# Kernel tuning notes

Hardware: AMD Instinct MI355X
Metric: run time of the kernel (lower is better)

Reference implementation:

```python
import jax, jax.numpy as jnp
import numpy as np

N_WORD = 32000
N_CLASS = 5
N_HIDDEN = 32
T, B = 2048, 512

def setup_inputs() -> dict:
    key = jax.random.key(0)
    k_x, k_emb, k_w, k_b, k_cw, k_cb = jax.random.split(key, 6)
    x = jax.random.randint(k_x, (T, B), 0, N_WORD, dtype=jnp.int64 if jax.config.read('jax_enable_x64') else jnp.int32)
    s_emb = 1.0  # nn.Embedding default N(0,1)
    emb = jax.random.normal(k_emb, (N_WORD, N_HIDDEN), dtype=jnp.float32) * s_emb
    # nn.Linear default init: U(-1/sqrt(fan_in), 1/sqrt(fan_in))
    lim_rnn = 1.0 / np.sqrt(2 * N_HIDDEN)
    W_rnn = jax.random.uniform(k_w, (2 * N_HIDDEN, N_HIDDEN), jnp.float32, -lim_rnn, lim_rnn)
    b_rnn = jax.random.uniform(k_b, (N_HIDDEN,), jnp.float32, -lim_rnn, lim_rnn)
    lim_cls = 1.0 / np.sqrt(N_HIDDEN)
    W_cls = jax.random.uniform(k_cw, (N_HIDDEN, N_CLASS), jnp.float32, -lim_cls, lim_cls)
    b_cls = jax.random.uniform(k_cb, (N_CLASS,), jnp.float32, -lim_cls, lim_cls)
    return {"x": x, "emb": emb, "W_rnn": W_rnn, "b_rnn": b_rnn, "W_cls": W_cls, "b_cls": b_cls}

def reference(x, emb, W_rnn, b_rnn, W_cls, b_cls):
    # x: [T, B] int token ids. Embed -> [T, B, H]
    xe = emb[x]
    # Split W_rnn into the part applied to x_t and the part applied to h
    # (cat([xt, h]) @ W == xt @ W[:H] + h @ W[H:]), avoids per-step concat.
    Wx, Wh = W_rnn[:N_HIDDEN], W_rnn[N_HIDDEN:]
    h0 = jnp.zeros((x.shape[1], N_HIDDEN), dtype=emb.dtype)

    def step(h, xt):
        h = jnp.tanh(xt @ Wx + h @ Wh + b_rnn)
        return h, None

    h_final, _ = jax.lax.scan(step, h0, xe)
    y = h_final @ W_cls + b_cls  # [B, n_class]
    return y
```

## Files before the change

### kernel.cpp

```cpp
#include <hip/hip_runtime.h>
#include <hip/hip_bf16.h>

#define TT 2048
#define BB 512
#define HH 32
#define NPAIR (TT * BB)
#define PSTRIDE (BB * HH)
#define CSC 2.88539008177792681f

#define PIN(x) asm volatile("" : "+v"(x))

#if defined(__has_builtin)
#  if __has_builtin(__builtin_amdgcn_permlane16_swap)
#    define HAVE_PLSWAP 1
#  endif
#endif
#ifndef HAVE_PLSWAP
#  define HAVE_PLSWAP 0
#endif

__device__ __forceinline__ float fast_tanh_pre(float u) {
    float e = exp2f(u);
    return fmaf(__builtin_amdgcn_rcpf(e + 1.0f), -2.0f, 1.0f);
}
__device__ __forceinline__ float fast_tanh(float u) {
    float e = exp2f(u * CSC);
    return fmaf(__builtin_amdgcn_rcpf(e + 1.0f), -2.0f, 1.0f);
}

template <int N>
__device__ __forceinline__ float dpp_ror(float v) {
    return __int_as_float(__builtin_amdgcn_mov_dpp(
        __float_as_int(v), 0x120 | N, 0xF, 0xF, false));
}
__device__ __forceinline__ float swz_x16(float v) {
    return __int_as_float(__builtin_amdgcn_ds_swizzle(__float_as_int(v), 0x401F));
}

__device__ __forceinline__ unsigned short f2bfu(float f) {
    __hip_bfloat16 h = __float2bfloat16(f);
    return *reinterpret_cast<unsigned short*>(&h);
}
__device__ __forceinline__ short f2bf(float f) {
    __hip_bfloat16 h = __float2bfloat16(f);
    return *reinterpret_cast<short*>(&h);
}

typedef __attribute__((ext_vector_type(8))) short bf16x8;
typedef __attribute__((ext_vector_type(4))) float f32x4;

__global__ __launch_bounds__(256) void precompute_mfma2(
        const int* __restrict__ x, const float* __restrict__ emb,
        const float* __restrict__ W_rnn, const float* __restrict__ b_rnn,
        __hip_bfloat16* __restrict__ P) {
    const int l  = threadIdx.x & 63;
    const int wv = (blockIdx.x * 256 + threadIdx.x) >> 6;
    const int m16 = l & 15;
    const int q   = l >> 4;
    const int pair0 = wv * 64;

    bf16x8 a0, a1;
#pragma unroll
    for (int j = 0; j < 8; ++j) {
        a0[j] = f2bf(CSC * W_rnn[(q * 8 + j) * HH + m16]);
        a1[j] = f2bf(CSC * W_rnn[(q * 8 + j) * HH + m16 + 16]);
    }
    f32x4 cb0, cb1;
#pragma unroll
    for (int reg = 0; reg < 4; ++reg) {
        cb0[reg] = CSC * b_rnn[q * 4 + reg];
        cb1[reg] = CSC * b_rnn[q * 4 + reg + 16];
    }

#pragma unroll
    for (int it = 0; it < 4; ++it) {
        const int pairB = pair0 + it * 16;
        const int idx = x[pairB + m16];
        const float4* ep = (const float4*)(emb + (size_t)idx * HH + q * 8);
        float4 e0 = ep[0], e1 = ep[1];
        bf16x8 bf;
        bf[0] = f2bf(e0.x); bf[1] = f2bf(e0.y); bf[2] = f2bf(e0.z); bf[3] = f2bf(e0.w);
        bf[4] = f2bf(e1.x); bf[5] = f2bf(e1.y); bf[6] = f2bf(e1.z); bf[7] = f2bf(e1.w);

        f32x4 c0 = cb0, c1 = cb1;
        c0 = __builtin_amdgcn_mfma_f32_16x16x32_bf16(a0, bf, c0, 0, 0, 0);
        c1 = __builtin_amdgcn_mfma_f32_16x16x32_bf16(a1, bf, c1, 0, 0, 0);

        uint2 s0, s1;
        s0.x = (unsigned)f2bfu(c0[0]) | ((unsigned)f2bfu(c0[1]) << 16);
        s0.y = (unsigned)f2bfu(c0[2]) | ((unsigned)f2bfu(c0[3]) << 16);
        s1.x = (unsigned)f2bfu(c1[0]) | ((unsigned)f2bfu(c1[1]) << 16);
        s1.y = (unsigned)f2bfu(c1[2]) | ((unsigned)f2bfu(c1[3]) << 16);
        __hip_bfloat16* pp = P + (size_t)(pairB + m16) * HH + q * 4;
        *(uint2*)(pp)      = s0;
        *(uint2*)(pp + 16) = s1;
    }
}

__global__ __launch_bounds__(64, 1) void rnn_seq_v14(
        const __hip_bfloat16* __restrict__ P, const float* __restrict__ W_rnn,
        const float* __restrict__ W_cls, const float* __restrict__ b_cls,
        float* __restrict__ out) {
    const int l = threadIdx.x;
    const int i = l & 15;
    const int q = (l >> 4) & 1;

    int rt = __builtin_amdgcn_mov_dpp(i, 0x121, 0xF, 0xF, false);
    const int d = (rt == ((i + 1) & 15)) ? 1 : -1;

#if HAVE_PLSWAP
    bool takeX;
    {
        unsigned lv = (unsigned)l;
        auto pr = __builtin_amdgcn_permlane16_swap(lv, lv, false, false);
        takeX = ((unsigned)pr[0] == (unsigned)(l ^ 16));
    }
#endif

    float wKeep[16], wSend[16];
#pragma unroll
    for (int o = 0; o < 16; ++o) {
        const int k = q * 16 + ((i + d * o) & 15);
        wKeep[o] = CSC * W_rnn[(HH + k) * HH + (q * 16 + i)];
        wSend[o] = CSC * W_rnn[(HH + k) * HH + ((q ^ 1) * 16 + i)];
    }
#pragma unroll
    for (int o = 0; o < 16; ++o) { PIN(wKeep[o]); PIN(wSend[o]); }

    const __hip_bfloat16* gp = P + (size_t)blockIdx.x * 64 + l;

    float pA[8], pB[8];
#pragma unroll
    for (int t = 0; t < 8; ++t)
        pA[t] = __bfloat162float(gp[(size_t)t * PSTRIDE]);

    float h = 0.0f;

    auto step = [&](float p) {
        float rot[16];
        rot[0] = h;
        rot[1]  = dpp_ror<1>(h);  rot[2]  = dpp_ror<2>(h);  rot[3]  = dpp_ror<3>(h);
        rot[4]  = dpp_ror<4>(h);  rot[5]  = dpp_ror<5>(h);  rot[6]  = dpp_ror<6>(h);
        rot[7]  = dpp_ror<7>(h);  rot[8]  = dpp_ror<8>(h);  rot[9]  = dpp_ror<9>(h);
        rot[10] = dpp_ror<10>(h); rot[11] = dpp_ror<11>(h); rot[12] = dpp_ror<12>(h);
        rot[13] = dpp_ror<13>(h); rot[14] = dpp_ror<14>(h); rot[15] = dpp_ror<15>(h);

        float s0 = rot[0] * wSend[0], s1 = rot[1] * wSend[1];
        float s2 = rot[2] * wSend[2], s3 = rot[3] * wSend[3];
#pragma unroll
        for (int m = 1; m < 4; ++m) {
            s0 = fmaf(rot[4*m+0], wSend[4*m+0], s0);
            s1 = fmaf(rot[4*m+1], wSend[4*m+1], s1);
            s2 = fmaf(rot[4*m+2], wSend[4*m+2], s2);
            s3 = fmaf(rot[4*m+3], wSend[4*m+3], s3);
        }
        float send = (s0 + s1) + (s2 + s3);
#if HAVE_PLSWAP
        unsigned sv = __float_as_uint(send);
        auto rr = __builtin_amdgcn_permlane16_swap(sv, sv, false, false);
        float recv = takeX ? __uint_as_float((unsigned)rr[0])
                           : __uint_as_float((unsigned)rr[1]);
#else
        float recv = swz_x16(send);
#endif
        float k0 = fmaf(rot[0], wKeep[0], p), k1 = rot[1] * wKeep[1];
        float k2 = rot[2] * wKeep[2],         k3 = rot[3] * wKeep[3];
#pragma unroll
        for (int m = 1; m < 4; ++m) {
            k0 = fmaf(rot[4*m+0], wKeep[4*m+0], k0);
            k1 = fmaf(rot[4*m+1], wKeep[4*m+1], k1);
            k2 = fmaf(rot[4*m+2], wKeep[4*m+2], k2);
            k3 = fmaf(rot[4*m+3], wKeep[4*m+3], k3);
        }
        float u = ((k0 + k1) + (k2 + k3)) + recv;
        h = fast_tanh_pre(u);
    };

#pragma unroll 1
    for (int e = 0; e < TT / 16; ++e) {
        const int tB = e * 16 + 8;
#pragma unroll
        for (int t = 0; t < 8; ++t)
            pB[t] = __bfloat162float(gp[(size_t)(tB + t) * PSTRIDE]);
#pragma unroll
        for (int t = 0; t < 8; ++t) PIN(pA[t]);
#pragma unroll
        for (int s = 0; s < 8; ++s) step(pA[s]);

        int tA = e * 16 + 16;
        if (tA > TT - 8) tA = TT - 8;
#pragma unroll
        for (int t = 0; t < 8; ++t)
            pA[t] = __bfloat162float(gp[(size_t)(tA + t) * PSTRIDE]);
#pragma unroll
        for (int t = 0; t < 8; ++t) PIN(pB[t]);
#pragma unroll
        for (int s = 0; s < 8; ++s) step(pB[s]);
    }

    __shared__ float hf[64];
    hf[l] = h;
    if (l < 10) {
        const int rr = l / 5, c = l % 5;
        float acc = b_cls[c];
#pragma unroll
        for (int k = 0; k < 32; ++k)
            acc = fmaf(hf[rr * 32 + k], W_cls[k * 5 + c], acc);
        out[(blockIdx.x * 2 + rr) * 5 + c] = acc;
    }
}

__device__ __forceinline__ float rnn_step_fb(const float4 xt[8], const float wx[32],
                                             const float wh[32], float bj,
                                             float* hrow, int lane) {
    float u0 = 0.f, u1 = 0.f, u2 = 0.f, u3 = 0.f;
#pragma unroll
    for (int q = 0; q < 8; ++q) {
        u0 = fmaf(xt[q].x, wx[4*q+0], u0);
        u1 = fmaf(xt[q].y, wx[4*q+1], u1);
        u2 = fmaf(xt[q].z, wx[4*q+2], u2);
        u3 = fmaf(xt[q].w, wx[4*q+3], u3);
    }
    const float4* hp = (const float4*)hrow;
#pragma unroll
    for (int q = 0; q < 8; ++q) {
        float4 hv = hp[q];
        u0 = fmaf(hv.x, wh[4*q+0], u0);
        u1 = fmaf(hv.y, wh[4*q+1], u1);
        u2 = fmaf(hv.z, wh[4*q+2], u2);
        u3 = fmaf(hv.w, wh[4*q+3], u3);
    }
    float hn = fast_tanh(bj + ((u0 + u1) + (u2 + u3)));
    hrow[lane] = hn;
    return hn;
}

__global__ __launch_bounds__(64, 1) void rnn_seq_kernel(
        const int* __restrict__ x, const float* __restrict__ emb,
        const float* __restrict__ W_rnn, const float* __restrict__ b_rnn,
        const float* __restrict__ W_cls, const float* __restrict__ b_cls,
        float* __restrict__ out) {
    const int lane = threadIdx.x & 31;
    const int grp  = threadIdx.x >> 5;
    const int row  = blockIdx.x * 2 + grp;
    __shared__ float hbuf[2][HH];
    float wx[32], wh[32];
#pragma unroll
    for (int k = 0; k < 32; ++k) {
        wx[k] = W_rnn[k * HH + lane];
        wh[k] = W_rnn[(HH + k) * HH + lane];
    }
    const float bj = b_rnn[lane];
    hbuf[grp][lane] = 0.0f;
    float* hrow = &hbuf[grp][0];
    int i1 = x[1 * BB + row];
    float4 xcur[8], xnxt[8];
    {
        int i0 = x[0 * BB + row];
        const float4* ep = (const float4*)(emb + (size_t)i0 * HH);
#pragma unroll
        for (int q = 0; q < 8; ++q) xcur[q] = ep[q];
    }
    for (int t = 0; t < TT; t += 2) {
        int i2 = x[min(t + 2, TT - 1) * BB + row];
        {
            const float4* ep = (const float4*)(emb + (size_t)i1 * HH);
#pragma unroll
            for (int q = 0; q < 8; ++q) xnxt[q] = ep[q];
        }
        rnn_step_fb(xcur, wx, wh, bj, hrow, lane);
        i1 = x[min(t + 3, TT - 1) * BB + row];
        {
            const float4* ep = (const float4*)(emb + (size_t)i2 * HH);
#pragma unroll
            for (int q = 0; q < 8; ++q) xcur[q] = ep[q];
        }
        rnn_step_fb(xnxt, wx, wh, bj, hrow, lane);
    }
    if (lane < 5) {
        float acc = b_cls[lane];
#pragma unroll
        for (int k = 0; k < 32; ++k)
            acc = fmaf(hrow[k], W_cls[k * 5 + lane], acc);
        out[row * 5 + lane] = acc;
    }
}

extern "C" void kernel_launch(void* const* d_in, const int* in_sizes, int n_in,
                              void* d_out, int out_size, void* d_ws, size_t ws_size,
                              hipStream_t stream) {
    const int*   x     = (const int*)d_in[0];
    const float* emb   = (const float*)d_in[1];
    const float* W_rnn = (const float*)d_in[2];
    const float* b_rnn = (const float*)d_in[3];
    const float* W_cls = (const float*)d_in[4];
    const float* b_cls = (const float*)d_in[5];
    float* out = (float*)d_out;

    const size_t need16 = (size_t)NPAIR * HH * 2;
    if (ws_size >= need16) {
        __hip_bfloat16* P = (__hip_bfloat16*)d_ws;
        const int pre_blocks = NPAIR / 256;
        precompute_mfma2<<<pre_blocks, 256, 0, stream>>>(x, emb, W_rnn, b_rnn, P);
        rnn_seq_v14<<<BB / 2, 64, 0, stream>>>(P, W_rnn, W_cls, b_cls, out);
    } else {
        rnn_seq_kernel<<<BB / 2, 64, 0, stream>>>(x, emb, W_rnn, b_rnn, W_cls, b_cls, out);
    }
}
```

Baseline: 329.6 us.

## Recast recurrence on sigmoid state and swap hidden state across halves before matvec

Each step now carries r = 1/(1+e^u) in place of h = tanh, using h = 1 - 2r. The factor -2 is folded into the recurrent weights and the constant term into a per-lane bias WS added to the precomputed input. This removes the final fma in tanh. The cross-half exchange now moves the state r before the dot product rather than the partial sum after it, so the permlane swap can overlap the local-half FMAs and the two halves form two independent chains. Prefetch loads use inline global_load_ushort with an explicit vmcnt(8) wait and a sched barrier so the next batch of loads stays in flight while the current one is consumed.

```diff
diff --git a/kernel.cpp b/kernel.cpp
--- a/kernel.cpp
+++ b/kernel.cpp
@@ -36,6 +36,16 @@
 __device__ __forceinline__ float swz_x16(float v) {
     return __int_as_float(__builtin_amdgcn_ds_swizzle(__float_as_int(v), 0x401F));
 }
+
+__device__ __forceinline__ unsigned gload_u16(const __hip_bfloat16* a) {
+    unsigned r;
+    asm volatile("global_load_ushort %0, %1, off" : "=v"(r) : "v"(a));
+    return r;
+}
+#define VMWAIT8_FENCE() do { \
+    asm volatile("s_waitcnt vmcnt(8)"); \
+    __builtin_amdgcn_sched_barrier(0); \
+} while (0)
 
 __device__ __forceinline__ unsigned short f2bfu(float f) {
     __hip_bfloat16 h = __float2bfloat16(f);
@@ -97,13 +107,14 @@
     }
 }
 
-__global__ __launch_bounds__(64, 1) void rnn_seq_v14(
+__global__ __launch_bounds__(64, 1) void rnn_seq_v15(
         const __hip_bfloat16* __restrict__ P, const float* __restrict__ W_rnn,
         const float* __restrict__ W_cls, const float* __restrict__ b_cls,
         float* __restrict__ out) {
     const int l = threadIdx.x;
     const int i = l & 15;
     const int q = (l >> 4) & 1;
+    const int j = q * 16 + i;
 
     int rt = __builtin_amdgcn_mov_dpp(i, 0x121, 0xF, 0xF, false);
     const int d = (rt == ((i + 1) & 15)) ? 1 : -1;
@@ -117,89 +128,115 @@
     }
 #endif
 
-    float wKeep[16], wSend[16];
+    float w1[16], w2[16];
 #pragma unroll
     for (int o = 0; o < 16; ++o) {
-        const int k = q * 16 + ((i + d * o) & 15);
-        wKeep[o] = CSC * W_rnn[(HH + k) * HH + (q * 16 + i)];
-        wSend[o] = CSC * W_rnn[(HH + k) * HH + ((q ^ 1) * 16 + i)];
-    }
-#pragma unroll
-    for (int o = 0; o < 16; ++o) { PIN(wKeep[o]); PIN(wSend[o]); }
+        const int kp = (i + d * o) & 15;
+        w1[o] = -2.0f * CSC * W_rnn[(HH + q * 16 + kp) * HH + j];
+        w2[o] = -2.0f * CSC * W_rnn[(HH + (q ^ 1) * 16 + kp) * HH + j];
+    }
+#pragma unroll
+    for (int o = 0; o < 16; ++o) { PIN(w1[o]); PIN(w2[o]); }
+
+    float WS = 0.0f;
+#pragma unroll
+    for (int k = 0; k < HH; ++k) WS += W_rnn[(HH + k) * HH + j];
+    WS *= CSC;
 
     const __hip_bfloat16* gp = P + (size_t)blockIdx.x * 64 + l;
 
-    float pA[8], pB[8];
+    unsigned rA[8], rB[8];
 #pragma unroll
     for (int t = 0; t < 8; ++t)
-        pA[t] = __bfloat162float(gp[(size_t)t * PSTRIDE]);
-
-    float h = 0.0f;
+        rA[t] = gload_u16(gp + (size_t)t * PSTRIDE);
+
+    float r = 0.5f;
 
     auto step = [&](float p) {
-        float rot[16];
-        rot[0] = h;
-        rot[1]  = dpp_ror<1>(h);  rot[2]  = dpp_ror<2>(h);  rot[3]  = dpp_ror<3>(h);
-        rot[4]  = dpp_ror<4>(h);  rot[5]  = dpp_ror<5>(h);  rot[6]  = dpp_ror<6>(h);
-        rot[7]  = dpp_ror<7>(h);  rot[8]  = dpp_ror<8>(h);  rot[9]  = dpp_ror<9>(h);
-        rot[10] = dpp_ror<10>(h); rot[11] = dpp_ror<11>(h); rot[12] = dpp_ror<12>(h);
-        rot[13] = dpp_ror<13>(h); rot[14] = dpp_ror<14>(h); rot[15] = dpp_ror<15>(h);
-
-        float s0 = rot[0] * wSend[0], s1 = rot[1] * wSend[1];
-        float s2 = rot[2] * wSend[2], s3 = rot[3] * wSend[3];
-#pragma unroll
-        for (int m = 1; m < 4; ++m) {
-            s0 = fmaf(rot[4*m+0], wSend[4*m+0], s0);
-            s1 = fmaf(rot[4*m+1], wSend[4*m+1], s1);
-            s2 = fmaf(rot[4*m+2], wSend[4*m+2], s2);
-            s3 = fmaf(rot[4*m+3], wSend[4*m+3], s3);
-        }
-        float send = (s0 + s1) + (s2 + s3);
 #if HAVE_PLSWAP
-        unsigned sv = __float_as_uint(send);
-        auto rr = __builtin_amdgcn_permlane16_swap(sv, sv, false, false);
-        float recv = takeX ? __uint_as_float((unsigned)rr[0])
-                           : __uint_as_float((unsigned)rr[1]);
+        unsigned rv = __float_as_uint(r);
+        auto sw = __builtin_amdgcn_permlane16_swap(rv, rv, false, false);
+        float rm = takeX ? __uint_as_float((unsigned)sw[0])
+                         : __uint_as_float((unsigned)sw[1]);
 #else
-        float recv = swz_x16(send);
+        float rm = swz_x16(r);
 #endif
-        float k0 = fmaf(rot[0], wKeep[0], p), k1 = rot[1] * wKeep[1];
-        float k2 = rot[2] * wKeep[2],         k3 = rot[3] * wKeep[3];
-#pragma unroll
-        for (int m = 1; m < 4; ++m) {
-            k0 = fmaf(rot[4*m+0], wKeep[4*m+0], k0);
-            k1 = fmaf(rot[4*m+1], wKeep[4*m+1], k1);
-            k2 = fmaf(rot[4*m+2], wKeep[4*m+2], k2);
-            k3 = fmaf(rot[4*m+3], wKeep[4*m+3], k3);
-        }
-        float u = ((k0 + k1) + (k2 + k3)) + recv;
-        h = fast_tanh_pre(u);
+        float a0 = fmaf(r,             w1[0], p);
+        float a1 = dpp_ror<1>(r)  * w1[1];
+        float a2 = dpp_ror<2>(r)  * w1[2];
+        float a3 = dpp_ror<3>(r)  * w1[3];
+        a0 = fmaf(dpp_ror<4>(r),  w1[4],  a0);
+        a1 = fmaf(dpp_ror<5>(r),  w1[5],  a1);
+        a2 = fmaf(dpp_ror<6>(r),  w1[6],  a2);
+        a3 = fmaf(dpp_ror<7>(r),  w1[7],  a3);
+        a0 = fmaf(dpp_ror<8>(r),  w1[8],  a0);
+        a1 = fmaf(dpp_ror<9>(r),  w1[9],  a1);
+        a2 = fmaf(dpp_ror<10>(r), w1[10], a2);
+        a3 = fmaf(dpp_ror<11>(r), w1[11], a3);
+        a0 = fmaf(dpp_ror<12>(r), w1[12], a0);
+        a1 = fmaf(dpp_ror<13>(r), w1[13], a1);
+        a2 = fmaf(dpp_ror<14>(r), w1[14], a2);
+        a3 = fmaf(dpp_ror<15>(r), w1[15], a3);
+
+        float a4 = rm             * w2[0];
+        float a5 = dpp_ror<1>(rm)  * w2[1];
+        float a6 = dpp_ror<2>(rm)  * w2[2];
+        float a7 = dpp_ror<3>(rm)  * w2[3];
+        a4 = fmaf(dpp_ror<4>(rm),  w2[4],  a4);
+        a5 = fmaf(dpp_ror<5>(rm),  w2[5],  a5);
+        a6 = fmaf(dpp_ror<6>(rm),  w2[6],  a6);
+        a7 = fmaf(dpp_ror<7>(rm),  w2[7],  a7);
+        a4 = fmaf(dpp_ror<8>(rm),  w2[8],  a4);
+        a5 = fmaf(dpp_ror<9>(rm),  w2[9],  a5);
+        a6 = fmaf(dpp_ror<10>(rm), w2[10], a6);
+        a7 = fmaf(dpp_ror<11>(rm), w2[11], a7);
+        a4 = fmaf(dpp_ror<12>(rm), w2[12], a4);
+        a5 = fmaf(dpp_ror<13>(rm), w2[13], a5);
+        a6 = fmaf(dpp_ror<14>(rm), w2[14], a6);
+        a7 = fmaf(dpp_ror<15>(rm), w2[15], a7);
+
+        float u = ((a0 + a1) + (a2 + a3)) + ((a4 + a5) + (a6 + a7));
+        float e = exp2f(u);
+        r = __builtin_amdgcn_rcpf(e + 1.0f);
     };
 
 #pragma unroll 1
     for (int e = 0; e < TT / 16; ++e) {
-        const int tB = e * 16 + 8;
-#pragma unroll
-        for (int t = 0; t < 8; ++t)
-            pB[t] = __bfloat162float(gp[(size_t)(tB + t) * PSTRIDE]);
-#pragma unroll
-        for (int t = 0; t < 8; ++t) PIN(pA[t]);
-#pragma unroll
-        for (int s = 0; s < 8; ++s) step(pA[s]);
-
-        int tA = e * 16 + 16;
-        if (tA > TT - 8) tA = TT - 8;
-#pragma unroll
-        for (int t = 0; t < 8; ++t)
-            pA[t] = __bfloat162float(gp[(size_t)(tA + t) * PSTRIDE]);
-#pragma unroll
-        for (int t = 0; t < 8; ++t) PIN(pB[t]);
-#pragma unroll
-        for (int s = 0; s < 8; ++s) step(pB[s]);
+        {
+            const int tB = e * 16 + 8;
+#pragma unroll
+            for (int t = 0; t < 8; ++t)
+                rB[t] = gload_u16(gp + (size_t)(tB + t) * PSTRIDE);
+        }
+        VMWAIT8_FENCE();
+        {
+            float p[8];
+#pragma unroll
+            for (int t = 0; t < 8; ++t)
+                p[t] = __uint_as_float(rA[t] << 16) + WS;
+#pragma unroll
+            for (int s = 0; s < 8; ++s) step(p[s]);
+        }
+        {
+            int tA = e * 16 + 16;
+            if (tA > TT - 8) tA = TT - 8;
+#pragma unroll
+            for (int t = 0; t < 8; ++t)
+                rA[t] = gload_u16(gp + (size_t)(tA + t) * PSTRIDE);
+        }
+        VMWAIT8_FENCE();
+        {
+            float p[8];
+#pragma unroll
+            for (int t = 0; t < 8; ++t)
+                p[t] = __uint_as_float(rB[t] << 16) + WS;
+#pragma unroll
+            for (int s = 0; s < 8; ++s) step(p[s]);
+        }
     }
 
     __shared__ float hf[64];
-    hf[l] = h;
+    hf[l] = fmaf(r, -2.0f, 1.0f);
     if (l < 10) {
         const int rr = l / 5, c = l % 5;
         float acc = b_cls[c];
@@ -302,7 +339,7 @@
         __hip_bfloat16* P = (__hip_bfloat16*)d_ws;
         const int pre_blocks = NPAIR / 256;
         precompute_mfma2<<<pre_blocks, 256, 0, stream>>>(x, emb, W_rnn, b_rnn, P);
-        rnn_seq_v14<<<BB / 2, 64, 0, stream>>>(P, W_rnn, W_cls, b_cls, out);
+        rnn_seq_v15<<<BB / 2, 64, 0, stream>>>(P, W_rnn, W_cls, b_cls, out);
     } else {
         rnn_seq_kernel<<<BB / 2, 64, 0, stream>>>(x, emb, W_rnn, b_rnn, W_cls, b_cls, out);
     }
```

Result: slower. 382.5 us (+16.1%).

## Interleave two independent batch-row recurrences per wave and fold tanh affine into weights

Applied to the files above, without the earlier changes.

Each wavefront now carries two independent pairs of batch rows through the recurrence, interleaving their DPP rotations, FMAs and cross-half swaps. This hides the latency of the serial dependency chain by giving the scheduler independent work, and halves the number of blocks. The tanh output's -2r+1 affine form is folded algebraically into the weights and a per-column bias, so each step only computes the reciprocal. The cost is more live registers and fewer waves across the device (128 blocks).

```diff
diff --git a/kernel.cpp b/kernel.cpp
--- a/kernel.cpp
+++ b/kernel.cpp
@@ -19,10 +19,6 @@
 #  define HAVE_PLSWAP 0
 #endif
 
-__device__ __forceinline__ float fast_tanh_pre(float u) {
-    float e = exp2f(u);
-    return fmaf(__builtin_amdgcn_rcpf(e + 1.0f), -2.0f, 1.0f);
-}
 __device__ __forceinline__ float fast_tanh(float u) {
     float e = exp2f(u * CSC);
     return fmaf(__builtin_amdgcn_rcpf(e + 1.0f), -2.0f, 1.0f);
@@ -97,13 +93,14 @@
     }
 }
 
-__global__ __launch_bounds__(64, 1) void rnn_seq_v14(
+__global__ __launch_bounds__(64, 1) void rnn_seq_v17(
         const __hip_bfloat16* __restrict__ P, const float* __restrict__ W_rnn,
         const float* __restrict__ W_cls, const float* __restrict__ b_cls,
         float* __restrict__ out) {
     const int l = threadIdx.x;
     const int i = l & 15;
     const int q = (l >> 4) & 1;
+    const int j = q * 16 + i;
 
     int rt = __builtin_amdgcn_mov_dpp(i, 0x121, 0xF, 0xF, false);
     const int d = (rt == ((i + 1) & 15)) ? 1 : -1;
@@ -117,96 +114,143 @@
     }
 #endif
 
-    float wKeep[16], wSend[16];
+    float wK[16], wS[16];
 #pragma unroll
     for (int o = 0; o < 16; ++o) {
         const int k = q * 16 + ((i + d * o) & 15);
-        wKeep[o] = CSC * W_rnn[(HH + k) * HH + (q * 16 + i)];
-        wSend[o] = CSC * W_rnn[(HH + k) * HH + ((q ^ 1) * 16 + i)];
-    }
-#pragma unroll
-    for (int o = 0; o < 16; ++o) { PIN(wKeep[o]); PIN(wSend[o]); }
-
-    const __hip_bfloat16* gp = P + (size_t)blockIdx.x * 64 + l;
-
-    float pA[8], pB[8];
-#pragma unroll
-    for (int t = 0; t < 8; ++t)
-        pA[t] = __bfloat162float(gp[(size_t)t * PSTRIDE]);
-
-    float h = 0.0f;
-
-    auto step = [&](float p) {
-        float rot[16];
-        rot[0] = h;
-        rot[1]  = dpp_ror<1>(h);  rot[2]  = dpp_ror<2>(h);  rot[3]  = dpp_ror<3>(h);
-        rot[4]  = dpp_ror<4>(h);  rot[5]  = dpp_ror<5>(h);  rot[6]  = dpp_ror<6>(h);
-        rot[7]  = dpp_ror<7>(h);  rot[8]  = dpp_ror<8>(h);  rot[9]  = dpp_ror<9>(h);
-        rot[10] = dpp_ror<10>(h); rot[11] = dpp_ror<11>(h); rot[12] = dpp_ror<12>(h);
-        rot[13] = dpp_ror<13>(h); rot[14] = dpp_ror<14>(h); rot[15] = dpp_ror<15>(h);
-
-        float s0 = rot[0] * wSend[0], s1 = rot[1] * wSend[1];
-        float s2 = rot[2] * wSend[2], s3 = rot[3] * wSend[3];
+        wK[o] = -2.0f * CSC * W_rnn[(HH + k) * HH + j];
+        wS[o] = -2.0f * CSC * W_rnn[(HH + k) * HH + ((q ^ 1) * 16 + i)];
+    }
+#pragma unroll
+    for (int o = 0; o < 16; ++o) { PIN(wK[o]); PIN(wS[o]); }
+
+    float WSf = 0.0f;
+#pragma unroll
+    for (int k = 0; k < HH; ++k) WSf += W_rnn[(HH + k) * HH + j];
+    WSf *= CSC;
+
+    const __hip_bfloat16* gp0 = P + (size_t)blockIdx.x * 128 + l;
+    const __hip_bfloat16* gp1 = gp0 + 64;
+
+    float pA0[8], pA1[8], pB0[8], pB1[8];
+#pragma unroll
+    for (int t = 0; t < 8; ++t) {
+        pA0[t] = __bfloat162float(gp0[(size_t)t * PSTRIDE]) + WSf;
+        pA1[t] = __bfloat162float(gp1[(size_t)t * PSTRIDE]) + WSf;
+    }
+
+    float r0 = 0.5f, r1 = 0.5f;
+
+    auto step2 = [&](float p0, float p1) {
+        float x0[16];
+        x0[0] = r0;
+        x0[1]  = dpp_ror<1>(r0);  x0[2]  = dpp_ror<2>(r0);  x0[3]  = dpp_ror<3>(r0);
+        x0[4]  = dpp_ror<4>(r0);  x0[5]  = dpp_ror<5>(r0);  x0[6]  = dpp_ror<6>(r0);
+        x0[7]  = dpp_ror<7>(r0);  x0[8]  = dpp_ror<8>(r0);  x0[9]  = dpp_ror<9>(r0);
+        x0[10] = dpp_ror<10>(r0); x0[11] = dpp_ror<11>(r0); x0[12] = dpp_ror<12>(r0);
+        x0[13] = dpp_ror<13>(r0); x0[14] = dpp_ror<14>(r0); x0[15] = dpp_ror<15>(r0);
+
+        float ka0 = fmaf(x0[0], wK[0], p0);
+        float ka1 = x0[1] * wK[1], ka2 = x0[2] * wK[2], ka3 = x0[3] * wK[3];
+        float sa0 = x0[0] * wS[0], sa1 = x0[1] * wS[1];
+        float sa2 = x0[2] * wS[2], sa3 = x0[3] * wS[3];
 #pragma unroll
         for (int m = 1; m < 4; ++m) {
-            s0 = fmaf(rot[4*m+0], wSend[4*m+0], s0);
-            s1 = fmaf(rot[4*m+1], wSend[4*m+1], s1);
-            s2 = fmaf(rot[4*m+2], wSend[4*m+2], s2);
-            s3 = fmaf(rot[4*m+3], wSend[4*m+3], s3);
-        }
-        float send = (s0 + s1) + (s2 + s3);
+            ka0 = fmaf(x0[4*m+0], wK[4*m+0], ka0);
+            ka1 = fmaf(x0[4*m+1], wK[4*m+1], ka1);
+            ka2 = fmaf(x0[4*m+2], wK[4*m+2], ka2);
+            ka3 = fmaf(x0[4*m+3], wK[4*m+3], ka3);
+            sa0 = fmaf(x0[4*m+0], wS[4*m+0], sa0);
+            sa1 = fmaf(x0[4*m+1], wS[4*m+1], sa1);
+            sa2 = fmaf(x0[4*m+2], wS[4*m+2], sa2);
+            sa3 = fmaf(x0[4*m+3], wS[4*m+3], sa3);
+        }
+        float send0 = (sa0 + sa1) + (sa2 + sa3);
 #if HAVE_PLSWAP
-        unsigned sv = __float_as_uint(send);
-        auto rr = __builtin_amdgcn_permlane16_swap(sv, sv, false, false);
-        float recv = takeX ? __uint_as_float((unsigned)rr[0])
-                           : __uint_as_float((unsigned)rr[1]);
+        unsigned sv0 = __float_as_uint(send0);
+        auto sw0 = __builtin_amdgcn_permlane16_swap(sv0, sv0, false, false);
+#endif
+
+        float x1[16];
+        x1[0] = r1;
+        x1[1]  = dpp_ror<1>(r1);  x1[2]  = dpp_ror<2>(r1);  x1[3]  = dpp_ror<3>(r1);
+        x1[4]  = dpp_ror<4>(r1);  x1[5]  = dpp_ror<5>(r1);  x1[6]  = dpp_ror<6>(r1);
+        x1[7]  = dpp_ror<7>(r1);  x1[8]  = dpp_ror<8>(r1);  x1[9]  = dpp_ror<9>(r1);
+        x1[10] = dpp_ror<10>(r1); x1[11] = dpp_ror<11>(r1); x1[12] = dpp_ror<12>(r1);
+        x1[13] = dpp_ror<13>(r1); x1[14] = dpp_ror<14>(r1); x1[15] = dpp_ror<15>(r1);
+
+        float kb0 = fmaf(x1[0], wK[0], p1);
+        float kb1 = x1[1] * wK[1], kb2 = x1[2] * wK[2], kb3 = x1[3] * wK[3];
+        float sb0 = x1[0] * wS[0], sb1 = x1[1] * wS[1];
+        float sb2 = x1[2] * wS[2], sb3 = x1[3] * wS[3];
+#pragma unroll
+        for (int m = 1; m < 4; ++m) {
+            kb0 = fmaf(x1[4*m+0], wK[4*m+0], kb0);
+            kb1 = fmaf(x1[4*m+1], wK[4*m+1], kb1);
+            kb2 = fmaf(x1[4*m+2], wK[4*m+2], kb2);
+            kb3 = fmaf(x1[4*m+3], wK[4*m+3], kb3);
+            sb0 = fmaf(x1[4*m+0], wS[4*m+0], sb0);
+            sb1 = fmaf(x1[4*m+1], wS[4*m+1], sb1);
+            sb2 = fmaf(x1[4*m+2], wS[4*m+2], sb2);
+            sb3 = fmaf(x1[4*m+3], wS[4*m+3], sb3);
+        }
+        float send1 = (sb0 + sb1) + (sb2 + sb3);
+#if HAVE_PLSWAP
+        unsigned sv1 = __float_as_uint(send1);
+        auto sw1 = __builtin_amdgcn_permlane16_swap(sv1, sv1, false, false);
+        float recv0 = takeX ? __uint_as_float((unsigned)sw0[0])
+                            : __uint_as_float((unsigned)sw0[1]);
+        float recv1 = takeX ? __uint_as_float((unsigned)sw1[0])
+                            : __uint_as_float((unsigned)sw1[1]);
 #else
-        float recv = swz_x16(send);
-#endif
-        float k0 = fmaf(rot[0], wKeep[0], p), k1 = rot[1] * wKeep[1];
-        float k2 = rot[2] * wKeep[2],         k3 = rot[3] * wKeep[3];
-#pragma unroll
-        for (int m = 1; m < 4; ++m) {
-            k0 = fmaf(rot[4*m+0], wKeep[4*m+0], k0);
-            k1 = fmaf(rot[4*m+1], wKeep[4*m+1], k1);
-            k2 = fmaf(rot[4*m+2], wKeep[4*m+2], k2);
-            k3 = fmaf(rot[4*m+3], wKeep[4*m+3], k3);
-        }
-        float u = ((k0 + k1) + (k2 + k3)) + recv;
-        h = fast_tanh_pre(u);
+        float recv0 = swz_x16(send0);
+        float recv1 = swz_x16(send1);
+#endif
+
+        float u0 = ((ka0 + ka1) + (ka2 + ka3)) + recv0;
+        float u1 = ((kb0 + kb1) + (kb2 + kb3)) + recv1;
+        float e0 = exp2f(u0);
+        float e1 = exp2f(u1);
+        r0 = __builtin_amdgcn_rcpf(e0 + 1.0f);
+        r1 = __builtin_amdgcn_rcpf(e1 + 1.0f);
     };
 
 #pragma unroll 1
     for (int e = 0; e < TT / 16; ++e) {
         const int tB = e * 16 + 8;
 #pragma unroll
-        for (int t = 0; t < 8; ++t)
-            pB[t] = __bfloat162float(gp[(size_t)(tB + t) * PSTRIDE]);
-#pragma unroll
-        for (int t = 0; t < 8; ++t) PIN(pA[t]);
-#pragma unroll
-        for (int s = 0; s < 8; ++s) step(pA[s]);
+        for (int t = 0; t < 8; ++t) {
+            pB0[t] = __bfloat162float(gp0[(size_t)(tB + t) * PSTRIDE]) + WSf;
+            pB1[t] = __bfloat162float(gp1[(size_t)(tB + t) * PSTRIDE]) + WSf;
+        }
+#pragma unroll
+        for (int t = 0; t < 8; ++t) { PIN(pA0[t]); PIN(pA1[t]); }
+#pragma unroll
+        for (int s = 0; s < 8; ++s) step2(pA0[s], pA1[s]);
 
         int tA = e * 16 + 16;
         if (tA > TT - 8) tA = TT - 8;
 #pragma unroll
-        for (int t = 0; t < 8; ++t)
-            pA[t] = __bfloat162float(gp[(size_t)(tA + t) * PSTRIDE]);
-#pragma unroll
-        for (int t = 0; t < 8; ++t) PIN(pB[t]);
-#pragma unroll
-        for (int s = 0; s < 8; ++s) step(pB[s]);
-    }
-
-    __shared__ float hf[64];
-    hf[l] = h;
-    if (l < 10) {
+        for (int t = 0; t < 8; ++t) {
+            pA0[t] = __bfloat162float(gp0[(size_t)(tA + t) * PSTRIDE]) + WSf;
+            pA1[t] = __bfloat162float(gp1[(size_t)(tA + t) * PSTRIDE]) + WSf;
+        }
+#pragma unroll
+        for (int t = 0; t < 8; ++t) { PIN(pB0[t]); PIN(pB1[t]); }
+#pragma unroll
+        for (int s = 0; s < 8; ++s) step2(pB0[s], pB1[s]);
+    }
+
+    __shared__ float hf[128];
+    hf[l]      = fmaf(r0, -2.0f, 1.0f);
+    hf[64 + l] = fmaf(r1, -2.0f, 1.0f);
+    if (l < 20) {
         const int rr = l / 5, c = l % 5;
         float acc = b_cls[c];
 #pragma unroll
         for (int k = 0; k < 32; ++k)
             acc = fmaf(hf[rr * 32 + k], W_cls[k * 5 + c], acc);
-        out[(blockIdx.x * 2 + rr) * 5 + c] = acc;
+        out[(blockIdx.x * 4 + rr) * 5 + c] = acc;
     }
 }
 
@@ -302,7 +346,7 @@
         __hip_bfloat16* P = (__hip_bfloat16*)d_ws;
         const int pre_blocks = NPAIR / 256;
         precompute_mfma2<<<pre_blocks, 256, 0, stream>>>(x, emb, W_rnn, b_rnn, P);
-        rnn_seq_v14<<<BB / 2, 64, 0, stream>>>(P, W_rnn, W_cls, b_cls, out);
+        rnn_seq_v17<<<BB / 4, 64, 0, stream>>>(P, W_rnn, W_cls, b_cls, out);
     } else {
         rnn_seq_kernel<<<BB / 2, 64, 0, stream>>>(x, emb, W_rnn, b_rnn, W_cls, b_cls, out);
     }
```

Result: slower. 518.0 us (+57.2%).

## Split each batch row's hidden state across a full wave with alternating permlane exchange

Applied to the files above, without the earlier changes.

The recurrent kernel now gives each 64-lane wave one batch row instead of two, splitting the 32x32 recurrence into four 16x16 quadrants. Even and odd timesteps use different quadrant assignments, exchanged via permlane16_swap and permlane32_swap respectively. Folding the -2 scale and a row-sum bias term into the weights lets each step carry r = 1/(1+e^u) and skip the tanh fma. It also launches twice as many blocks (BB instead of BB/2) to expose more parallelism and shorten the per-step dependency chain. The cost is doubled global loads of the precomputed projections and reliance on the more complex remapping being correct.

```diff
diff --git a/kernel.cpp b/kernel.cpp
--- a/kernel.cpp
+++ b/kernel.cpp
@@ -12,17 +12,19 @@
 
 #if defined(__has_builtin)
 #  if __has_builtin(__builtin_amdgcn_permlane16_swap)
-#    define HAVE_PLSWAP 1
+#    define HAVE_PL16 1
 #  endif
-#endif
-#ifndef HAVE_PLSWAP
-#  define HAVE_PLSWAP 0
-#endif
-
-__device__ __forceinline__ float fast_tanh_pre(float u) {
-    float e = exp2f(u);
-    return fmaf(__builtin_amdgcn_rcpf(e + 1.0f), -2.0f, 1.0f);
-}
+#  if __has_builtin(__builtin_amdgcn_permlane32_swap)
+#    define HAVE_PL32 1
+#  endif
+#endif
+#ifndef HAVE_PL16
+#  define HAVE_PL16 0
+#endif
+#ifndef HAVE_PL32
+#  define HAVE_PL32 0
+#endif
+
 __device__ __forceinline__ float fast_tanh(float u) {
     float e = exp2f(u * CSC);
     return fmaf(__builtin_amdgcn_rcpf(e + 1.0f), -2.0f, 1.0f);
@@ -97,116 +99,171 @@
     }
 }
 
-__global__ __launch_bounds__(64, 1) void rnn_seq_v14(
+__global__ __launch_bounds__(64, 1) void rnn_seq_v18(
         const __hip_bfloat16* __restrict__ P, const float* __restrict__ W_rnn,
         const float* __restrict__ W_cls, const float* __restrict__ b_cls,
         float* __restrict__ out) {
     const int l = threadIdx.x;
     const int i = l & 15;
-    const int q = (l >> 4) & 1;
+    const int g = l >> 4;
 
     int rt = __builtin_amdgcn_mov_dpp(i, 0x121, 0xF, 0xF, false);
     const int d = (rt == ((i + 1) & 15)) ? 1 : -1;
 
-#if HAVE_PLSWAP
-    bool takeX;
+#if HAVE_PL16
+    bool takeX16;
     {
         unsigned lv = (unsigned)l;
         auto pr = __builtin_amdgcn_permlane16_swap(lv, lv, false, false);
-        takeX = ((unsigned)pr[0] == (unsigned)(l ^ 16));
-    }
-#endif
-
-    float wKeep[16], wSend[16];
+        takeX16 = ((unsigned)pr[0] == (unsigned)(l ^ 16));
+    }
+#endif
+#if HAVE_PL32
+    bool takeX32;
+    {
+        unsigned lv = (unsigned)l;
+        auto pr = __builtin_amdgcn_permlane32_swap(lv, lv, false, false);
+        takeX32 = ((unsigned)pr[0] == (unsigned)(l ^ 32));
+    }
+#endif
+
+    const int heldE = g & 1;
+    const int heldO = g >> 1;
+    const int jE = (g >> 1) * 16 + i;
+    const int jO = (g & 1) * 16 + i;
+
+    float wE[16], wO[16];
 #pragma unroll
     for (int o = 0; o < 16; ++o) {
-        const int k = q * 16 + ((i + d * o) & 15);
-        wKeep[o] = CSC * W_rnn[(HH + k) * HH + (q * 16 + i)];
-        wSend[o] = CSC * W_rnn[(HH + k) * HH + ((q ^ 1) * 16 + i)];
-    }
-#pragma unroll
-    for (int o = 0; o < 16; ++o) { PIN(wKeep[o]); PIN(wSend[o]); }
-
-    const __hip_bfloat16* gp = P + (size_t)blockIdx.x * 64 + l;
-
-    float pA[8], pB[8];
-#pragma unroll
-    for (int t = 0; t < 8; ++t)
-        pA[t] = __bfloat162float(gp[(size_t)t * PSTRIDE]);
-
-    float h = 0.0f;
-
-    auto step = [&](float p) {
+        const int kk = (i + d * o) & 15;
+        wE[o] = -2.0f * CSC * W_rnn[(HH + heldE * 16 + kk) * HH + jE];
+        wO[o] = -2.0f * CSC * W_rnn[(HH + heldO * 16 + kk) * HH + jO];
+    }
+#pragma unroll
+    for (int o = 0; o < 16; ++o) { PIN(wE[o]); PIN(wO[o]); }
+
+    float WSE = 0.0f, WSO = 0.0f;
+#pragma unroll
+    for (int k = 0; k < HH; ++k) {
+        WSE += W_rnn[(HH + k) * HH + jE];
+        WSO += W_rnn[(HH + k) * HH + jO];
+    }
+    const float mEf  = (heldE == 0) ? 1.0f : 0.0f;
+    const float wsbE = (heldE == 0) ? CSC * WSE : 0.0f;
+    const float mOf  = (heldO == 0) ? 1.0f : 0.0f;
+    const float wsbO = (heldO == 0) ? CSC * WSO : 0.0f;
+
+    const int row = blockIdx.x;
+    const __hip_bfloat16* gpE = P + (size_t)row * HH + jE;
+    const __hip_bfloat16* gpO = P + (size_t)row * HH + jO;
+
+    float peA[4], poA[4], peB[4], poB[4];
+#pragma unroll
+    for (int s = 0; s < 4; ++s) {
+        peA[s] = __bfloat162float(gpE[(size_t)(2 * s) * PSTRIDE]);
+        poA[s] = __bfloat162float(gpO[(size_t)(2 * s + 1) * PSTRIDE]);
+    }
+
+    float r = 0.5f;
+
+    auto stepE = [&](float pld) {
+        float p_eff = fmaf(pld, mEf, wsbE);
         float rot[16];
-        rot[0] = h;
-        rot[1]  = dpp_ror<1>(h);  rot[2]  = dpp_ror<2>(h);  rot[3]  = dpp_ror<3>(h);
-        rot[4]  = dpp_ror<4>(h);  rot[5]  = dpp_ror<5>(h);  rot[6]  = dpp_ror<6>(h);
-        rot[7]  = dpp_ror<7>(h);  rot[8]  = dpp_ror<8>(h);  rot[9]  = dpp_ror<9>(h);
-        rot[10] = dpp_ror<10>(h); rot[11] = dpp_ror<11>(h); rot[12] = dpp_ror<12>(h);
-        rot[13] = dpp_ror<13>(h); rot[14] = dpp_ror<14>(h); rot[15] = dpp_ror<15>(h);
-
-        float s0 = rot[0] * wSend[0], s1 = rot[1] * wSend[1];
-        float s2 = rot[2] * wSend[2], s3 = rot[3] * wSend[3];
+        rot[0] = r;
+        rot[1]  = dpp_ror<1>(r);  rot[2]  = dpp_ror<2>(r);  rot[3]  = dpp_ror<3>(r);
+        rot[4]  = dpp_ror<4>(r);  rot[5]  = dpp_ror<5>(r);  rot[6]  = dpp_ror<6>(r);
+        rot[7]  = dpp_ror<7>(r);  rot[8]  = dpp_ror<8>(r);  rot[9]  = dpp_ror<9>(r);
+        rot[10] = dpp_ror<10>(r); rot[11] = dpp_ror<11>(r); rot[12] = dpp_ror<12>(r);
+        rot[13] = dpp_ror<13>(r); rot[14] = dpp_ror<14>(r); rot[15] = dpp_ror<15>(r);
+        float c0 = fmaf(rot[0], wE[0], p_eff);
+        float c1 = rot[1] * wE[1], c2 = rot[2] * wE[2], c3 = rot[3] * wE[3];
 #pragma unroll
         for (int m = 1; m < 4; ++m) {
-            s0 = fmaf(rot[4*m+0], wSend[4*m+0], s0);
-            s1 = fmaf(rot[4*m+1], wSend[4*m+1], s1);
-            s2 = fmaf(rot[4*m+2], wSend[4*m+2], s2);
-            s3 = fmaf(rot[4*m+3], wSend[4*m+3], s3);
-        }
-        float send = (s0 + s1) + (s2 + s3);
-#if HAVE_PLSWAP
-        unsigned sv = __float_as_uint(send);
-        auto rr = __builtin_amdgcn_permlane16_swap(sv, sv, false, false);
-        float recv = takeX ? __uint_as_float((unsigned)rr[0])
-                           : __uint_as_float((unsigned)rr[1]);
+            c0 = fmaf(rot[4*m+0], wE[4*m+0], c0);
+            c1 = fmaf(rot[4*m+1], wE[4*m+1], c1);
+            c2 = fmaf(rot[4*m+2], wE[4*m+2], c2);
+            c3 = fmaf(rot[4*m+3], wE[4*m+3], c3);
+        }
+        float own = (c0 + c1) + (c2 + c3);
+#if HAVE_PL16
+        unsigned sv = __float_as_uint(own);
+        auto sw = __builtin_amdgcn_permlane16_swap(sv, sv, false, false);
+        float recv = takeX16 ? __uint_as_float((unsigned)sw[0])
+                             : __uint_as_float((unsigned)sw[1]);
 #else
-        float recv = swz_x16(send);
-#endif
-        float k0 = fmaf(rot[0], wKeep[0], p), k1 = rot[1] * wKeep[1];
-        float k2 = rot[2] * wKeep[2],         k3 = rot[3] * wKeep[3];
+        float recv = swz_x16(own);
+#endif
+        float u = own + recv;
+        float e = exp2f(u);
+        r = __builtin_amdgcn_rcpf(e + 1.0f);
+    };
+
+    auto stepO = [&](float pld) {
+        float p_eff = fmaf(pld, mOf, wsbO);
+        float rot[16];
+        rot[0] = r;
+        rot[1]  = dpp_ror<1>(r);  rot[2]  = dpp_ror<2>(r);  rot[3]  = dpp_ror<3>(r);
+        rot[4]  = dpp_ror<4>(r);  rot[5]  = dpp_ror<5>(r);  rot[6]  = dpp_ror<6>(r);
+        rot[7]  = dpp_ror<7>(r);  rot[8]  = dpp_ror<8>(r);  rot[9]  = dpp_ror<9>(r);
+        rot[10] = dpp_ror<10>(r); rot[11] = dpp_ror<11>(r); rot[12] = dpp_ror<12>(r);
+        rot[13] = dpp_ror<13>(r); rot[14] = dpp_ror<14>(r); rot[15] = dpp_ror<15>(r);
+        float c0 = fmaf(rot[0], wO[0], p_eff);
+        float c1 = rot[1] * wO[1], c2 = rot[2] * wO[2], c3 = rot[3] * wO[3];
 #pragma unroll
         for (int m = 1; m < 4; ++m) {
-            k0 = fmaf(rot[4*m+0], wKeep[4*m+0], k0);
-            k1 = fmaf(rot[4*m+1], wKeep[4*m+1], k1);
-            k2 = fmaf(rot[4*m+2], wKeep[4*m+2], k2);
-            k3 = fmaf(rot[4*m+3], wKeep[4*m+3], k3);
-        }
-        float u = ((k0 + k1) + (k2 + k3)) + recv;
-        h = fast_tanh_pre(u);
+            c0 = fmaf(rot[4*m+0], wO[4*m+0], c0);
+            c1 = fmaf(rot[4*m+1], wO[4*m+1], c1);
+            c2 = fmaf(rot[4*m+2], wO[4*m+2], c2);
+            c3 = fmaf(rot[4*m+3], wO[4*m+3], c3);
+        }
+        float own = (c0 + c1) + (c2 + c3);
+#if HAVE_PL32
+        unsigned sv = __float_as_uint(own);
+        auto sw = __builtin_amdgcn_permlane32_swap(sv, sv, false, false);
+        float recv = takeX32 ? __uint_as_float((unsigned)sw[0])
+                             : __uint_as_float((unsigned)sw[1]);
+#else
+        float recv = __shfl_xor(own, 32, 64);
+#endif
+        float u = own + recv;
+        float e = exp2f(u);
+        r = __builtin_amdgcn_rcpf(e + 1.0f);
     };
 
 #pragma unroll 1
     for (int e = 0; e < TT / 16; ++e) {
         const int tB = e * 16 + 8;
 #pragma unroll
-        for (int t = 0; t < 8; ++t)
-            pB[t] = __bfloat162float(gp[(size_t)(tB + t) * PSTRIDE]);
-#pragma unroll
-        for (int t = 0; t < 8; ++t) PIN(pA[t]);
-#pragma unroll
-        for (int s = 0; s < 8; ++s) step(pA[s]);
+        for (int s = 0; s < 4; ++s) {
+            peB[s] = __bfloat162float(gpE[(size_t)(tB + 2 * s) * PSTRIDE]);
+            poB[s] = __bfloat162float(gpO[(size_t)(tB + 2 * s + 1) * PSTRIDE]);
+        }
+#pragma unroll
+        for (int s = 0; s < 4; ++s) { PIN(peA[s]); PIN(poA[s]); }
+#pragma unroll
+        for (int s = 0; s < 4; ++s) { stepE(peA[s]); stepO(poA[s]); }
 
         int tA = e * 16 + 16;
         if (tA > TT - 8) tA = TT - 8;
 #pragma unroll
-        for (int t = 0; t < 8; ++t)
-            pA[t] = __bfloat162float(gp[(size_t)(tA + t) * PSTRIDE]);
-#pragma unroll
-        for (int t = 0; t < 8; ++t) PIN(pB[t]);
-#pragma unroll
-        for (int s = 0; s < 8; ++s) step(pB[s]);
-    }
-
-    __shared__ float hf[64];
-    hf[l] = h;
-    if (l < 10) {
-        const int rr = l / 5, c = l % 5;
-        float acc = b_cls[c];
+        for (int s = 0; s < 4; ++s) {
+            peA[s] = __bfloat162float(gpE[(size_t)(tA + 2 * s) * PSTRIDE]);
+            poA[s] = __bfloat162float(gpO[(size_t)(tA + 2 * s + 1) * PSTRIDE]);
+        }
+#pragma unroll
+        for (int s = 0; s < 4; ++s) { PIN(peB[s]); PIN(poB[s]); }
+#pragma unroll
+        for (int s = 0; s < 4; ++s) { stepE(peB[s]); stepO(poB[s]); }
+    }
+
+    __shared__ float hf[32];
+    if (l < 32) hf[l] = fmaf(r, -2.0f, 1.0f);
+    if (l < 5) {
+        float acc = b_cls[l];
 #pragma unroll
         for (int k = 0; k < 32; ++k)
-            acc = fmaf(hf[rr * 32 + k], W_cls[k * 5 + c], acc);
-        out[(blockIdx.x * 2 + rr) * 5 + c] = acc;
+            acc = fmaf(hf[k], W_cls[k * 5 + l], acc);
+        out[row * 5 + l] = acc;
     }
 }
 
@@ -302,7 +359,7 @@
         __hip_bfloat16* P = (__hip_bfloat16*)d_ws;
         const int pre_blocks = NPAIR / 256;
         precompute_mfma2<<<pre_blocks, 256, 0, stream>>>(x, emb, W_rnn, b_rnn, P);
-        rnn_seq_v14<<<BB / 2, 64, 0, stream>>>(P, W_rnn, W_cls, b_cls, out);
+        rnn_seq_v18<<<BB, 64, 0, stream>>>(P, W_rnn, W_cls, b_cls, out);
     } else {
         rnn_seq_kernel<<<BB / 2, 64, 0, stream>>>(x, emb, W_rnn, b_rnn, W_cls, b_cls, out);
     }
```

New measurement: 664.4 us. +101.6%, slower.
